# Kernel optimization log

Measured on AMD Instinct MI355X. Metric: run time of the kernel, lower is better.

Reference implementation:

```python
import jax, jax.numpy as jnp
import numpy as np

B, S, E, H, ML = 4, 1024, 1024, 16, 2048
HD = E // H


def setup_inputs() -> dict:
    key = jax.random.key(0)
    ks = jax.random.split(key, 8)
    s = 0.02
    return {
        "x": jax.random.normal(ks[0], (B, S, E), dtype=jnp.float32),
        "rel_pos": jax.random.normal(ks[1], (H, ML), dtype=jnp.float32),
        "in_proj_w": jax.random.normal(ks[2], (3 * E, E), dtype=jnp.float32) * s,
        "in_proj_b": jnp.zeros((3 * E,), jnp.float32),
        "out_w": jax.random.normal(ks[3], (E, E), dtype=jnp.float32) * s,
        "out_b": jnp.zeros((E,), jnp.float32),
        "w1": jax.random.normal(ks[4], (4 * E, E), dtype=jnp.float32) * s,
        "b1": jnp.zeros((4 * E,), jnp.float32),
        "w2": jax.random.normal(ks[5], (E, 4 * E), dtype=jnp.float32) * s,
        "b2": jnp.zeros((E,), jnp.float32),
        "ln1_g": jnp.ones((E,), jnp.float32),
        "ln1_b": jnp.zeros((E,), jnp.float32),
        "ln2_g": jnp.ones((E,), jnp.float32),
        "ln2_b": jnp.zeros((E,), jnp.float32),
    }


def _layernorm(x, g, b, eps=1e-5):
    m = x.mean(-1, keepdims=True)
    v = ((x - m) ** 2).mean(-1, keepdims=True)
    return (x - m) * jax.lax.rsqrt(v + eps) * g + b


def _causal_mask(size, rel_pos):
    # rel_pos: [H, max_len]; size <= max_len branch of the torch code
    flipped = jnp.flip(rel_pos[:, :size], -1)                        # [H, size]
    neg_inf = jnp.full((rel_pos.shape[0], size), -jnp.inf, rel_pos.dtype)
    padded = jnp.concatenate([flipped, neg_inf], axis=-1)            # [H, 2*size]
    idx = jnp.arange(size)[None, :] - jnp.arange(size)[:, None] + size - 1
    return padded[:, idx]                                            # [H, S, S]: rel_pos[i-j] if j<=i else -inf


def reference(x, rel_pos, in_proj_w, in_proj_b, out_w, out_b,
              w1, b1, w2, b2, ln1_g, ln1_b, ln2_g, ln2_b):
    b, s, e = x.shape
    xn = _layernorm(x, ln1_g, ln1_b)
    qkv = xn @ in_proj_w.T + in_proj_b                               # [B,S,3E]
    q, k, v = jnp.split(qkv, 3, axis=-1)
    q = q.reshape(b, s, H, HD).transpose(0, 2, 1, 3)                 # [B,H,S,D]
    k = k.reshape(b, s, H, HD).transpose(0, 2, 1, 3)
    v = v.reshape(b, s, H, HD).transpose(0, 2, 1, 3)
    mask = _causal_mask(s, rel_pos)                                  # [H,S,S], broadcast over batch (== repeat(B,1,1))
    scores = jnp.einsum("bhqd,bhkd->bhqk", q, k) / np.sqrt(HD) + mask[None]
    attn = jax.nn.softmax(scores, axis=-1)
    o = jnp.einsum("bhqk,bhkd->bhqd", attn, v)                       # [B,H,S,D]
    o = o.transpose(0, 2, 1, 3).reshape(b, s, e)
    att_out = o @ out_w.T + out_b
    x = x + att_out
    xm = _layernorm(x, ln2_g, ln2_b)
    mlp = jax.nn.relu(xm @ w1.T + b1) @ w2.T + b2
    return x + mlp
```

## Files before the change

### kernel.cpp

```cpp
#include <hip/hip_runtime.h>
#include <stdint.h>

typedef __bf16 bf16x8 __attribute__((ext_vector_type(8)));
typedef float  f32x4  __attribute__((ext_vector_type(4)));

__device__ __forceinline__ unsigned short f2bf(float f) {
  union { float f; unsigned int u; } a; a.f = f;
  unsigned int r = a.u + 0x7FFFu + ((a.u >> 16) & 1u);
  return (unsigned short)(r >> 16);
}

__device__ __forceinline__ unsigned short f2bf_fast(float f) {
  union { __bf16 b; unsigned short u; } v; v.b = (__bf16)f; return v.u;
}

__device__ __forceinline__ void cp16(const void* g, void* l) {
  auto g1 = reinterpret_cast<__attribute__((address_space(1))) unsigned int*>(
      reinterpret_cast<uintptr_t>(g));
  auto l3 = reinterpret_cast<__attribute__((address_space(3))) unsigned int*>(
      reinterpret_cast<uintptr_t>(l));
  __builtin_amdgcn_global_load_lds(g1, l3, 16, 0, 0);
}

__global__ __launch_bounds__(256) void cvt_bf16(const float* __restrict__ in,
                                                unsigned short* __restrict__ out,
                                                int n) {
  int i = (blockIdx.x * 256 + threadIdx.x) * 4;
  if (i >= n) return;
  float4 v = *(const float4*)(in + i);
  union { unsigned short u[4]; uint2 p; } o;
  o.u[0] = f2bf(v.x); o.u[1] = f2bf(v.y); o.u[2] = f2bf(v.z); o.u[3] = f2bf(v.w);
  *(uint2*)(out + i) = o.p;
}

__global__ __launch_bounds__(256) void ln_bf16(const float* __restrict__ x,
                                               const float* __restrict__ g,
                                               const float* __restrict__ bta,
                                               unsigned short* __restrict__ out) {
  const int row = blockIdx.x, t = threadIdx.x;
  const float4 v = *(const float4*)(x + (size_t)row * 1024 + t * 4);
  float s1 = v.x + v.y + v.z + v.w;
  float s2 = v.x*v.x + v.y*v.y + v.z*v.z + v.w*v.w;
  #pragma unroll
  for (int off = 1; off < 64; off <<= 1) {
    s1 += __shfl_xor(s1, off, 64);
    s2 += __shfl_xor(s2, off, 64);
  }
  __shared__ float r1[4], r2[4];
  if ((t & 63) == 0) { r1[t >> 6] = s1; r2[t >> 6] = s2; }
  __syncthreads();
  s1 = r1[0] + r1[1] + r1[2] + r1[3];
  s2 = r2[0] + r2[1] + r2[2] + r2[3];
  const float mean = s1 * (1.0f / 1024.0f);
  const float var  = s2 * (1.0f / 1024.0f) - mean * mean;
  const float rstd = rsqrtf(var + 1e-5f);
  const float4 gv = *(const float4*)(g + t * 4);
  const float4 bv = *(const float4*)(bta + t * 4);
  union { unsigned short u[4]; uint2 p; } o;
  o.u[0] = f2bf((v.x - mean) * rstd * gv.x + bv.x);
  o.u[1] = f2bf((v.y - mean) * rstd * gv.y + bv.y);
  o.u[2] = f2bf((v.z - mean) * rstd * gv.z + bv.z);
  o.u[3] = f2bf((v.w - mean) * rstd * gv.w + bv.w);
  *(uint2*)(out + (size_t)row * 1024 + t * 4) = o.p;
}

template <int MODE>
__global__ __launch_bounds__(256, 2) void gemm_bt(
    const unsigned short* __restrict__ A,
    const unsigned short* __restrict__ Bt,
    const float* __restrict__ bias,
    const float* __restrict__ resid,
    void* __restrict__ outp,
    int N, int K) {
  __shared__ __align__(16) unsigned short As[128 * 64];
  __shared__ __align__(16) unsigned short Bs[128 * 64];
  const int tid = threadIdx.x;
  const int wave = tid >> 6, lane = tid & 63;
  const int q = lane >> 4, c = lane & 15;
  const int wm = (wave & 1) << 6, wn = (wave >> 1) << 6;
  const int m0 = blockIdx.x << 7, n0 = blockIdx.y << 7;

  const int srow = tid >> 3;
  const int cg8  = ((tid & 7) ^ (srow & 7)) << 3;

  const unsigned short* gA = A  + (size_t)(m0 + srow) * K + cg8;
  const unsigned short* gB = Bt + (size_t)(n0 + srow) * K + cg8;
  unsigned short* lA = &As[tid * 8];
  unsigned short* lB = &Bs[tid * 8];
  const size_t rstep = (size_t)32 * K;

  const f32x4 fzero = {0.f, 0.f, 0.f, 0.f};
  f32x4 acc[4][4];
  #pragma unroll
  for (int i = 0; i < 4; i++)
    #pragma unroll
    for (int j = 0; j < 4; j++) acc[i][j] = fzero;

  for (int k0 = 0; k0 < K; k0 += 64) {
    __syncthreads();
    #pragma unroll
    for (int it = 0; it < 4; it++) {
      cp16(gA + it * rstep + k0, lA + it * 2048);
      cp16(gB + it * rstep + k0, lB + it * 2048);
    }
    __syncthreads();
    #pragma unroll
    for (int ks = 0; ks < 2; ks++) {
      const int sw = (((ks << 2) + q) ^ (c & 7)) << 3;
      bf16x8 af[4], bf[4];
      #pragma unroll
      for (int i = 0; i < 4; i++) af[i] = *(const bf16x8*)&As[(wm + i*16 + c)*64 + sw];
      #pragma unroll
      for (int j = 0; j < 4; j++) bf[j] = *(const bf16x8*)&Bs[(wn + j*16 + c)*64 + sw];
      #pragma unroll
      for (int i = 0; i < 4; i++)
        #pragma unroll
        for (int j = 0; j < 4; j++)
          acc[i][j] = __builtin_amdgcn_mfma_f32_16x16x32_bf16(af[i], bf[j], acc[i][j], 0, 0, 0);
    }
  }

  float bj[4];
  #pragma unroll
  for (int j = 0; j < 4; j++) bj[j] = bias[n0 + wn + j * 16 + c];
  #pragma unroll
  for (int i = 0; i < 4; i++) {
    #pragma unroll
    for (int r = 0; r < 4; r++) {
      const int row = m0 + wm + i * 16 + q * 4 + r;
      #pragma unroll
      for (int j = 0; j < 4; j++) {
        const int col = n0 + wn + j * 16 + c;
        const size_t idx = (size_t)row * N + col;
        float v = acc[i][j][r] + bj[j];
        if (MODE == 0)      ((unsigned short*)outp)[idx] = f2bf(v);
        else if (MODE == 1) ((float*)outp)[idx] = v + resid[idx];
        else if (MODE == 2) ((unsigned short*)outp)[idx] = f2bf(fmaxf(v, 0.f));
        else                ((float*)outp)[idx] = v + resid[idx];
      }
    }
  }
}

__global__ __launch_bounds__(256, 2) void attn_flash(
    const unsigned short* __restrict__ qkv,
    const float* __restrict__ rel_pos,
    unsigned short* __restrict__ o) {
  __shared__ __align__(16) unsigned short Qs[128 * 64];
  __shared__ __align__(16) unsigned short Ks[64 * 64];
  __shared__ __align__(16) unsigned short Vs[64 * 64];
  __shared__ __align__(16) unsigned short Ps[4][32 * 64];
  __shared__ float rps[1024];

  const int tid = threadIdx.x;
  const int wave = tid >> 6, lane = tid & 63;
  const int q = lane >> 4, c = lane & 15;

  const int lid = blockIdx.x + (blockIdx.y << 3);
  const int xq = lid & 7, y = lid >> 3;
  const int qt = (y & 32) ? (7 - xq) : xq;
  const int b = y >> 4, h = y & 15;

  const unsigned short* qg = qkv + (size_t)b * 1024 * 3072 + h * 64;
  const unsigned short* kg = qg + 1024;
  const unsigned short* vg = qg + 2048;

  #pragma unroll
  for (int i = 0; i < 4; i++) {
    const int idx = tid + i * 256;
    rps[idx & 1023] = rel_pos[h * 2048 + (idx & 1023)] * 1.44269504f;
  }

  const int sr  = tid >> 3;
  const int cg8 = ((tid & 7) ^ (sr & 7)) << 3;
  #pragma unroll
  for (int it = 0; it < 4; it++)
    cp16(qg + (size_t)(qt * 128 + sr + it * 32) * 3072 + cg8, &Qs[(tid + it * 256) * 8]);
  __syncthreads();

  bf16x8 qf[2][2];
  #pragma unroll
  for (int mt = 0; mt < 2; mt++)
    #pragma unroll
    for (int ks = 0; ks < 2; ks++)
      qf[mt][ks] = *(const bf16x8*)&Qs[(wave*32 + mt*16 + c)*64 + ((((ks<<2)+q) ^ (c & 7)) << 3)];

  const f32x4 fzero = {0.f, 0.f, 0.f, 0.f};
  f32x4 O[2][4];
  float l_i[2][4];
  #pragma unroll
  for (int mt = 0; mt < 2; mt++) {
    #pragma unroll
    for (int r = 0; r < 4; r++) l_i[mt][r] = 0.f;
    #pragma unroll
    for (int dt = 0; dt < 4; dt++) O[mt][dt] = fzero;
  }

  unsigned short* Pw = &Ps[wave][0];
  const int i_base = qt * 128 + wave * 32;
  const int vrow = tid & 63, d0 = (tid >> 6) << 4;
  const int vchunk = vrow >> 3, vlo = vrow & 7;

  const float sc = 0.125f * 1.44269504f;
  const int kdiag = qt << 1;
  const int nkt = (qt + 1) * 2;

  for (int kt = 0; kt < nkt; kt++) {
    __syncthreads();
    cp16(kg + (size_t)(kt * 64 + sr) * 3072 + cg8, &Ks[tid * 8]);
    cp16(kg + (size_t)(kt * 64 + sr + 32) * 3072 + cg8, &Ks[(tid + 256) * 8]);
    {
      union { int4 v; unsigned short u[8]; } va, vb2;
      const unsigned short* vrp = vg + (size_t)(kt * 64 + vrow) * 3072 + d0;
      va.v  = *(const int4*)vrp;
      vb2.v = *(const int4*)(vrp + 8);
      #pragma unroll
      for (int j = 0; j < 8; j++) {
        const int pos = ((vchunk ^ j) << 3) + vlo;
        Vs[(d0 + j) * 64 + pos]     = va.u[j];
        Vs[(d0 + 8 + j) * 64 + pos] = vb2.u[j];
      }
    }
    __syncthreads();

    f32x4 S[2][4];
    #pragma unroll
    for (int mt = 0; mt < 2; mt++)
      #pragma unroll
      for (int nt = 0; nt < 4; nt++) S[mt][nt] = fzero;
    #pragma unroll
    for (int ks = 0; ks < 2; ks++) {
      const int sw = (((ks << 2) + q) ^ (c & 7)) << 3;
      bf16x8 kb[4];
      #pragma unroll
      for (int nt = 0; nt < 4; nt++) kb[nt] = *(const bf16x8*)&Ks[(nt*16 + c)*64 + sw];
      #pragma unroll
      for (int mt = 0; mt < 2; mt++)
        #pragma unroll
        for (int nt = 0; nt < 4; nt++)
          S[mt][nt] = __builtin_amdgcn_mfma_f32_16x16x32_bf16(qf[mt][ks], kb[nt], S[mt][nt], 0, 0, 0);
    }

    if (kt < kdiag) {
      #pragma unroll
      for (int mt = 0; mt < 2; mt++) {
        #pragma unroll
        for (int r = 0; r < 4; r++) {
          const int i_ = i_base + mt * 16 + q * 4 + r;
          const int prow = (mt * 16 + q * 4 + r) * 64;
          const int rsw  = (q * 4 + r) & 7;
          float s = 0.f;
          #pragma unroll
          for (int nt = 0; nt < 4; nt++) {
            const int j_ = kt * 64 + nt * 16 + c;
            const float p = exp2f(fmaf(S[mt][nt][r], sc, rps[i_ - j_]));
            s += p;
            Pw[prow + ((((nt << 1) + (c >> 3)) ^ rsw) << 3) + (c & 7)] = f2bf_fast(p);
          }
          l_i[mt][r] += s;
        }
      }
    } else {
      #pragma unroll
      for (int mt = 0; mt < 2; mt++) {
        #pragma unroll
        for (int r = 0; r < 4; r++) {
          const int i_ = i_base + mt * 16 + q * 4 + r;
          const int prow = (mt * 16 + q * 4 + r) * 64;
          const int rsw  = (q * 4 + r) & 7;
          float s = 0.f;
          #pragma unroll
          for (int nt = 0; nt < 4; nt++) {
            const int j_ = kt * 64 + nt * 16 + c;
            const int d_ = i_ - j_;
            const float p = (d_ >= 0)
                ? exp2f(fmaf(S[mt][nt][r], sc, rps[d_ & 1023])) : 0.f;
            s += p;
            Pw[prow + ((((nt << 1) + (c >> 3)) ^ rsw) << 3) + (c & 7)] = f2bf_fast(p);
          }
          l_i[mt][r] += s;
        }
      }
    }

    asm volatile("s_waitcnt lgkmcnt(0)" ::: "memory");

    #pragma unroll
    for (int ks = 0; ks < 2; ks++) {
      const int sw = (((ks << 2) + q) ^ (c & 7)) << 3;
      bf16x8 pa[2], vb[4];
      #pragma unroll
      for (int mt = 0; mt < 2; mt++) pa[mt] = *(const bf16x8*)&Pw[(mt*16 + c)*64 + sw];
      #pragma unroll
      for (int dt = 0; dt < 4; dt++) vb[dt] = *(const bf16x8*)&Vs[(dt*16 + c)*64 + sw];
      #pragma unroll
      for (int mt = 0; mt < 2; mt++)
        #pragma unroll
        for (int dt = 0; dt < 4; dt++)
          O[mt][dt] = __builtin_amdgcn_mfma_f32_16x16x32_bf16(pa[mt], vb[dt], O[mt][dt], 0, 0, 0);
    }
  }

  #pragma unroll
  for (int mt = 0; mt < 2; mt++) {
    #pragma unroll
    for (int r = 0; r < 4; r++) {
      float l = l_i[mt][r];
      l += __shfl_xor(l, 1, 64);
      l += __shfl_xor(l, 2, 64);
      l += __shfl_xor(l, 4, 64);
      l += __shfl_xor(l, 8, 64);
      const float inv = 1.0f / l;
      const int i_ = i_base + mt * 16 + q * 4 + r;
      unsigned short* orow = o + (size_t)(b * 1024 + i_) * 1024 + h * 64 + c;
      #pragma unroll
      for (int dt = 0; dt < 4; dt++) orow[dt * 16] = f2bf(O[mt][dt][r] * inv);
    }
  }
}

extern "C" void kernel_launch(void* const* d_in, const int* in_sizes, int n_in,
                              void* d_out, int out_size, void* d_ws, size_t ws_size,
                              hipStream_t stream) {
  (void)in_sizes; (void)n_in; (void)out_size; (void)ws_size;
  const float* x    = (const float*)d_in[0];
  const float* rel  = (const float*)d_in[1];
  const float* ipw  = (const float*)d_in[2];
  const float* ipb  = (const float*)d_in[3];
  const float* outw = (const float*)d_in[4];
  const float* outb = (const float*)d_in[5];
  const float* w1   = (const float*)d_in[6];
  const float* b1   = (const float*)d_in[7];
  const float* w2   = (const float*)d_in[8];
  const float* b2   = (const float*)d_in[9];
  const float* ln1g = (const float*)d_in[10];
  const float* ln1b = (const float*)d_in[11];
  const float* ln2g = (const float*)d_in[12];
  const float* ln2b = (const float*)d_in[13];

  unsigned short* ipw_b  = (unsigned short*)d_ws;
  unsigned short* outw_b = ipw_b  + (size_t)3072 * 1024;
  unsigned short* w1_b   = outw_b + (size_t)1024 * 1024;
  unsigned short* w2_b   = w1_b   + (size_t)4096 * 1024;
  unsigned short* xn     = w2_b   + (size_t)1024 * 4096;
  unsigned short* qkvb   = xn     + (size_t)4096 * 1024;
  unsigned short* ob     = qkvb   + (size_t)4096 * 3072;
  float*          x2     = (float*)(ob + (size_t)4096 * 1024);
  unsigned short* xm     = (unsigned short*)(x2 + (size_t)4096 * 1024);
  unsigned short* hb     = xm + (size_t)4096 * 1024;

  cvt_bf16<<<3072 * 1024 / 1024, 256, 0, stream>>>(ipw, ipw_b, 3072 * 1024);
  cvt_bf16<<<1024 * 1024 / 1024, 256, 0, stream>>>(outw, outw_b, 1024 * 1024);
  cvt_bf16<<<4096 * 1024 / 1024, 256, 0, stream>>>(w1, w1_b, 4096 * 1024);
  cvt_bf16<<<4096 * 1024 / 1024, 256, 0, stream>>>(w2, w2_b, 4096 * 1024);

  ln_bf16<<<4096, 256, 0, stream>>>(x, ln1g, ln1b, xn);

  gemm_bt<0><<<dim3(32, 24), 256, 0, stream>>>(xn, ipw_b, ipb, nullptr, qkvb, 3072, 1024);

  attn_flash<<<dim3(8, 64), 256, 0, stream>>>(qkvb, rel, ob);

  gemm_bt<1><<<dim3(32, 8), 256, 0, stream>>>(ob, outw_b, outb, x, x2, 1024, 1024);

  ln_bf16<<<4096, 256, 0, stream>>>(x2, ln2g, ln2b, xm);

  gemm_bt<2><<<dim3(32, 32), 256, 0, stream>>>(xm, w1_b, b1, nullptr, hb, 4096, 1024);

  gemm_bt<3><<<dim3(32, 8), 256, 0, stream>>>(hb, w2_b, b2, x2, (float*)d_out, 1024, 4096);
}
```

Baseline: 341.6 us.

## Split-K the two N=1024 GEMMs with atomic accumulation into pre-initialized residual

The out-projection and MLP down-projection GEMMs, which only launched 256 tiles, now run as split-K over two halves of K, giving 512 blocks to fill the GPU better. Outputs are pre-initialized with residual plus bias by a new elementwise kernel, and partial sums are accumulated with float atomicAdd. The trade-off is an extra pass over the output, atomic traffic in the epilogue, and fp32 summation order that can vary between runs.

```diff
diff --git a/kernel.cpp b/kernel.cpp
--- a/kernel.cpp
+++ b/kernel.cpp
@@ -31,6 +31,16 @@
   union { unsigned short u[4]; uint2 p; } o;
   o.u[0] = f2bf(v.x); o.u[1] = f2bf(v.y); o.u[2] = f2bf(v.z); o.u[3] = f2bf(v.w);
   *(uint2*)(out + i) = o.p;
+}
+
+__global__ __launch_bounds__(256) void init_br(const float* __restrict__ resid,
+                                               const float* __restrict__ bias,
+                                               float* __restrict__ out) {
+  int i = (blockIdx.x * 256 + threadIdx.x) * 4;
+  float4 r = *(const float4*)(resid + i);
+  float4 b = *(const float4*)(bias + (i & 1023));
+  r.x += b.x; r.y += b.y; r.z += b.z; r.w += b.w;
+  *(float4*)(out + i) = r;
 }
 
 __global__ __launch_bounds__(256) void ln_bf16(const float* __restrict__ x,
@@ -69,7 +79,6 @@
     const unsigned short* __restrict__ A,
     const unsigned short* __restrict__ Bt,
     const float* __restrict__ bias,
-    const float* __restrict__ resid,
     void* __restrict__ outp,
     int N, int K) {
   __shared__ __align__(16) unsigned short As[128 * 64];
@@ -134,9 +143,76 @@
         const size_t idx = (size_t)row * N + col;
         float v = acc[i][j][r] + bj[j];
         if (MODE == 0)      ((unsigned short*)outp)[idx] = f2bf(v);
-        else if (MODE == 1) ((float*)outp)[idx] = v + resid[idx];
-        else if (MODE == 2) ((unsigned short*)outp)[idx] = f2bf(fmaxf(v, 0.f));
-        else                ((float*)outp)[idx] = v + resid[idx];
+        else                ((unsigned short*)outp)[idx] = f2bf(fmaxf(v, 0.f));
+      }
+    }
+  }
+}
+
+__global__ __launch_bounds__(256, 2) void gemm_bt_splitk(
+    const unsigned short* __restrict__ A,
+    const unsigned short* __restrict__ Bt,
+    float* __restrict__ outp,
+    int N, int K) {
+  __shared__ __align__(16) unsigned short As[128 * 64];
+  __shared__ __align__(16) unsigned short Bs[128 * 64];
+  const int tid = threadIdx.x;
+  const int wave = tid >> 6, lane = tid & 63;
+  const int q = lane >> 4, c = lane & 15;
+  const int wm = (wave & 1) << 6, wn = (wave >> 1) << 6;
+  const int m0 = blockIdx.x << 7, n0 = blockIdx.y << 7;
+  const int KH = K >> 1;
+  const int kbeg = blockIdx.z * KH, kend = kbeg + KH;
+
+  const int srow = tid >> 3;
+  const int cg8  = ((tid & 7) ^ (srow & 7)) << 3;
+
+  const unsigned short* gA = A  + (size_t)(m0 + srow) * K + cg8;
+  const unsigned short* gB = Bt + (size_t)(n0 + srow) * K + cg8;
+  unsigned short* lA = &As[tid * 8];
+  unsigned short* lB = &Bs[tid * 8];
+  const size_t rstep = (size_t)32 * K;
+
+  const f32x4 fzero = {0.f, 0.f, 0.f, 0.f};
+  f32x4 acc[4][4];
+  #pragma unroll
+  for (int i = 0; i < 4; i++)
+    #pragma unroll
+    for (int j = 0; j < 4; j++) acc[i][j] = fzero;
+
+  for (int k0 = kbeg; k0 < kend; k0 += 64) {
+    __syncthreads();
+    #pragma unroll
+    for (int it = 0; it < 4; it++) {
+      cp16(gA + it * rstep + k0, lA + it * 2048);
+      cp16(gB + it * rstep + k0, lB + it * 2048);
+    }
+    __syncthreads();
+    #pragma unroll
+    for (int ks = 0; ks < 2; ks++) {
+      const int sw = (((ks << 2) + q) ^ (c & 7)) << 3;
+      bf16x8 af[4], bf[4];
+      #pragma unroll
+      for (int i = 0; i < 4; i++) af[i] = *(const bf16x8*)&As[(wm + i*16 + c)*64 + sw];
+      #pragma unroll
+      for (int j = 0; j < 4; j++) bf[j] = *(const bf16x8*)&Bs[(wn + j*16 + c)*64 + sw];
+      #pragma unroll
+      for (int i = 0; i < 4; i++)
+        #pragma unroll
+        for (int j = 0; j < 4; j++)
+          acc[i][j] = __builtin_amdgcn_mfma_f32_16x16x32_bf16(af[i], bf[j], acc[i][j], 0, 0, 0);
+    }
+  }
+
+  #pragma unroll
+  for (int i = 0; i < 4; i++) {
+    #pragma unroll
+    for (int r = 0; r < 4; r++) {
+      const int row = m0 + wm + i * 16 + q * 4 + r;
+      #pragma unroll
+      for (int j = 0; j < 4; j++) {
+        const int col = n0 + wn + j * 16 + c;
+        atomicAdd(outp + (size_t)row * N + col, acc[i][j][r]);
       }
     }
   }
@@ -356,15 +432,17 @@
 
   ln_bf16<<<4096, 256, 0, stream>>>(x, ln1g, ln1b, xn);
 
-  gemm_bt<0><<<dim3(32, 24), 256, 0, stream>>>(xn, ipw_b, ipb, nullptr, qkvb, 3072, 1024);
+  gemm_bt<0><<<dim3(32, 24), 256, 0, stream>>>(xn, ipw_b, ipb, qkvb, 3072, 1024);
 
   attn_flash<<<dim3(8, 64), 256, 0, stream>>>(qkvb, rel, ob);
 
-  gemm_bt<1><<<dim3(32, 8), 256, 0, stream>>>(ob, outw_b, outb, x, x2, 1024, 1024);
+  init_br<<<4096, 256, 0, stream>>>(x, outb, x2);
+  gemm_bt_splitk<<<dim3(32, 8, 2), 256, 0, stream>>>(ob, outw_b, x2, 1024, 1024);
 
   ln_bf16<<<4096, 256, 0, stream>>>(x2, ln2g, ln2b, xm);
 
-  gemm_bt<2><<<dim3(32, 32), 256, 0, stream>>>(xm, w1_b, b1, nullptr, hb, 4096, 1024);
-
-  gemm_bt<3><<<dim3(32, 8), 256, 0, stream>>>(hb, w2_b, b2, x2, (float*)d_out, 1024, 4096);
-}
+  gemm_bt<2><<<dim3(32, 32), 256, 0, stream>>>(xm, w1_b, b1, hb, 4096, 1024);
+
+  init_br<<<4096, 256, 0, stream>>>(x2, b2, (float*)d_out);
+  gemm_bt_splitk<<<dim3(32, 8, 2), 256, 0, stream>>>(hb, w2_b, (float*)d_out, 1024, 4096);
+}
```

After: 347.9 us. No clear change (+1.8%).
